# Performance work log

Hardware: AMD Instinct MI355X
Metric: run time of the kernel (lower is better)

## Reference

```python
import jax, jax.numpy as jnp
import numpy as np

INV_SQRT_2 = 0.7071067811865476


def setup_inputs() -> dict:
    key = jax.random.key(0)
    k1, k2, k3, k4, k5 = jax.random.split(key, 5)
    batch, nodes, edges, dim_in, dim_out = 2, 10000, 320000, 64, 64
    x = jax.random.normal(k1, (batch, nodes, dim_in, 3), dtype=jnp.float32)
    src = jax.random.randint(k2, (edges,), 0, nodes, dtype=jnp.int32)
    dst = jax.random.randint(k3, (edges,), 0, nodes, dtype=jnp.int32)
    # VecLinear weights (no bias; equivariant linear over the channel dim)
    W_src = jax.random.normal(k4, (dim_out, dim_in), dtype=jnp.float32) / np.sqrt(dim_in)
    W_dst = jax.random.normal(k5, (dim_out, dim_in), dtype=jnp.float32) / np.sqrt(dim_in)
    return {"x": x, "W_src": W_src, "W_dst": W_dst, "src": src, "dst": dst}


def reference(x, W_src, W_dst, src, dst):
    # x: (b, nodes, dim_in, 3); gather node feats per edge, mix channels, combine.
    xs = jnp.take(x, src, axis=1)  # (b, edges, dim_in, 3)
    xd = jnp.take(x, dst, axis=1)  # (b, edges, dim_in, 3)
    ys = jnp.einsum('oi,beiv->beov', W_src, xs)
    yd = jnp.einsum('oi,beiv->beov', W_dst, xd)
    return (ys + yd) * INV_SQRT_2  # (b, edges, dim_out, 3)
```

## Files before the change

kernel.cpp:

```cpp
#include <hip/hip_runtime.h>

#define INV_SQRT_2F 0.70710678118654752440f

typedef float fvec4 __attribute__((ext_vector_type(4)));

static __device__ __forceinline__ unsigned short f2bf(float f)
{
    unsigned int u = __float_as_uint(f);
    u += 0x7fffu + ((u >> 16) & 1u);
    return (unsigned short)(u >> 16);
}

static __device__ __forceinline__ fvec4 combine4(uint2 a, uint2 b)
{
    fvec4 r;
    r.x = (__uint_as_float(a.x << 16)         + __uint_as_float(b.x << 16))         * INV_SQRT_2F;
    r.y = (__uint_as_float(a.x & 0xffff0000u) + __uint_as_float(b.x & 0xffff0000u)) * INV_SQRT_2F;
    r.z = (__uint_as_float(a.y << 16)         + __uint_as_float(b.y << 16))         * INV_SQRT_2F;
    r.w = (__uint_as_float(a.y & 0xffff0000u) + __uint_as_float(b.y & 0xffff0000u)) * INV_SQRT_2F;
    return r;
}

__global__ void pack_sd(const int* __restrict__ src,
                        const int* __restrict__ dst,
                        unsigned int* __restrict__ sd, int edges)
{
    int i = blockIdx.x * blockDim.x + threadIdx.x;
    int stride = gridDim.x * blockDim.x;
    for (; i < edges; i += stride)
        sd[i] = ((unsigned int)src[i] << 16) | (unsigned int)dst[i];
}

__global__ void __launch_bounds__(128)
node_transform(const float* __restrict__ x,
               const float* __restrict__ W_src,
               const float* __restrict__ W_dst,
               unsigned short* __restrict__ y_src,
               unsigned short* __restrict__ y_dst,
               int nodes, int bn_total)
{
    __shared__ float xs[192];
    int bn = blockIdx.x;
    if (bn >= bn_total) return;
    int b = bn / nodes;
    int n = bn - b * nodes;

    const float4* xp = (const float4*)(x + (size_t)bn * 192);
    int t = threadIdx.x;
    if (t < 48) ((float4*)xs)[t] = xp[t];
    __syncthreads();

    int o = t & 63;
    const float*    W = (t < 64) ? W_src : W_dst;
    unsigned short* y = (t < 64) ? y_src : y_dst;

    const float4* Wrow = (const float4*)(W + o * 64);
    float a0 = 0.f, a1 = 0.f, a2 = 0.f;
#pragma unroll
    for (int i4 = 0; i4 < 16; ++i4) {
        float4 w = Wrow[i4];
        int i = i4 * 4;
        a0 = fmaf(w.x, xs[(i + 0) * 3 + 0], a0);
        a1 = fmaf(w.x, xs[(i + 0) * 3 + 1], a1);
        a2 = fmaf(w.x, xs[(i + 0) * 3 + 2], a2);
        a0 = fmaf(w.y, xs[(i + 1) * 3 + 0], a0);
        a1 = fmaf(w.y, xs[(i + 1) * 3 + 1], a1);
        a2 = fmaf(w.y, xs[(i + 1) * 3 + 2], a2);
        a0 = fmaf(w.z, xs[(i + 2) * 3 + 0], a0);
        a1 = fmaf(w.z, xs[(i + 2) * 3 + 1], a1);
        a2 = fmaf(w.z, xs[(i + 2) * 3 + 2], a2);
        a0 = fmaf(w.w, xs[(i + 3) * 3 + 0], a0);
        a1 = fmaf(w.w, xs[(i + 3) * 3 + 1], a1);
        a2 = fmaf(w.w, xs[(i + 3) * 3 + 2], a2);
    }
    unsigned short* yp = y + ((size_t)n * 2 + b) * 192 + o * 3;
    yp[0] = f2bf(a0);
    yp[1] = f2bf(a1);
    yp[2] = f2bf(a2);
}

__global__ void __launch_bounds__(256)
edge_combine2(const unsigned short* __restrict__ y_src,
              const unsigned short* __restrict__ y_dst,
              const unsigned int* __restrict__ sd,
              float* __restrict__ out,
              int edges)
{
    const int half   = edges >> 1;
    const int total  = half * 48;
    const int stride = gridDim.x * blockDim.x;
    const uint2* ys = (const uint2*)y_src;
    const uint2* yd = (const uint2*)y_dst;
    fvec4*       o4 = (fvec4*)out;

    for (int t = blockIdx.x * blockDim.x + threadIdx.x; t < total; t += stride) {
        int e0 = t / 48;
        int j  = t - e0 * 48;
        int e1 = e0 + half;

        unsigned int p0 = sd[e0];
        unsigned int p1 = sd[e1];
        size_t s0 = (size_t)(p0 >> 16)      * 96 + j;
        size_t d0 = (size_t)(p0 & 0xffffu)  * 96 + j;
        size_t s1 = (size_t)(p1 >> 16)      * 96 + j;
        size_t d1 = (size_t)(p1 & 0xffffu)  * 96 + j;

        uint2 a00 = ys[s0];
        uint2 b00 = yd[d0];
        uint2 a01 = ys[s0 + 48];
        uint2 b01 = yd[d0 + 48];
        uint2 a10 = ys[s1];
        uint2 b10 = yd[d1];
        uint2 a11 = ys[s1 + 48];
        uint2 b11 = yd[d1 + 48];

        __builtin_nontemporal_store(combine4(a00, b00), &o4[(size_t)e0 * 48 + j]);
        __builtin_nontemporal_store(combine4(a01, b01), &o4[((size_t)edges + e0) * 48 + j]);
        __builtin_nontemporal_store(combine4(a10, b10), &o4[(size_t)e1 * 48 + j]);
        __builtin_nontemporal_store(combine4(a11, b11), &o4[((size_t)edges + e1) * 48 + j]);
    }
}

__global__ void edge_combine_last(const unsigned short* __restrict__ y_src,
                                  const unsigned short* __restrict__ y_dst,
                                  const unsigned int* __restrict__ sd,
                                  float* __restrict__ out,
                                  int edges)
{
    int j = threadIdx.x;
    int e = edges - 1;
    const uint2* ys = (const uint2*)y_src;
    const uint2* yd = (const uint2*)y_dst;
    fvec4*       o4 = (fvec4*)out;
    unsigned int p = sd[e];
    size_t s = (size_t)(p >> 16)     * 96 + j;
    size_t d = (size_t)(p & 0xffffu) * 96 + j;
    uint2 a0 = ys[s];
    uint2 b0 = yd[d];
    uint2 a1 = ys[s + 48];
    uint2 b1 = yd[d + 48];
    __builtin_nontemporal_store(combine4(a0, b0), &o4[(size_t)e * 48 + j]);
    __builtin_nontemporal_store(combine4(a1, b1), &o4[((size_t)edges + e) * 48 + j]);
}

__global__ void __launch_bounds__(256)
edge_combine(const unsigned short* __restrict__ y_src,
             const unsigned short* __restrict__ y_dst,
             const int* __restrict__ src,
             const int* __restrict__ dst,
             float* __restrict__ out,
             int edges)
{
    const int total  = edges * 48;
    const int stride = gridDim.x * blockDim.x;
    const uint2* ys = (const uint2*)y_src;
    const uint2* yd = (const uint2*)y_dst;
    fvec4*       o4 = (fvec4*)out;

    for (int t = blockIdx.x * blockDim.x + threadIdx.x; t < total; t += stride) {
        int e = t / 48;
        int j = t - e * 48;
        size_t sb = (size_t)src[e] * 96 + j;
        size_t db = (size_t)dst[e] * 96 + j;

        uint2 a0 = ys[sb];
        uint2 b0 = yd[db];
        uint2 a1 = ys[sb + 48];
        uint2 b1 = yd[db + 48];

        __builtin_nontemporal_store(combine4(a0, b0), &o4[(size_t)e * 48 + j]);
        __builtin_nontemporal_store(combine4(a1, b1), &o4[((size_t)edges + e) * 48 + j]);
    }
}

__global__ void __launch_bounds__(64)
edge_fused(const float* __restrict__ x,
           const float* __restrict__ W_src,
           const float* __restrict__ W_dst,
           const int* __restrict__ src,
           const int* __restrict__ dst,
           float* __restrict__ out,
           int edges, int nodes)
{
    __shared__ float xs[192];
    __shared__ float xd[192];
    int be = blockIdx.x;
    int b  = be / edges;
    int e  = be - b * edges;
    int s  = src[e];
    int d  = dst[e];
    const float* xps = x + ((size_t)b * nodes + s) * 192;
    const float* xpd = x + ((size_t)b * nodes + d) * 192;
    int t = threadIdx.x;
#pragma unroll
    for (int k = 0; k < 3; ++k) {
        xs[t + 64 * k] = xps[t + 64 * k];
        xd[t + 64 * k] = xpd[t + 64 * k];
    }
    __syncthreads();
    float a0 = 0.f, a1 = 0.f, a2 = 0.f;
#pragma unroll
    for (int i = 0; i < 64; ++i) {
        float ws = W_src[t * 64 + i];
        float wd = W_dst[t * 64 + i];
        a0 += ws * xs[i * 3 + 0] + wd * xd[i * 3 + 0];
        a1 += ws * xs[i * 3 + 1] + wd * xd[i * 3 + 1];
        a2 += ws * xs[i * 3 + 2] + wd * xd[i * 3 + 2];
    }
    float* op = out + ((size_t)b * edges + e) * 192 + t * 3;
    op[0] = a0 * INV_SQRT_2F;
    op[1] = a1 * INV_SQRT_2F;
    op[2] = a2 * INV_SQRT_2F;
}

extern "C" void kernel_launch(void* const* d_in, const int* in_sizes, int n_in,
                              void* d_out, int out_size, void* d_ws, size_t ws_size,
                              hipStream_t stream)
{
    const float* x     = (const float*)d_in[0];
    const float* W_src = (const float*)d_in[1];
    const float* W_dst = (const float*)d_in[2];
    const int*   src   = (const int*)d_in[3];
    const int*   dst   = (const int*)d_in[4];
    float*       out   = (float*)d_out;

    const int batch = 2;
    const int edges = in_sizes[3];
    const int nodes = in_sizes[0] / (batch * 192);

    const size_t y_elems = (size_t)batch * nodes * 192;
    const size_t y_bytes = ((y_elems * 2 + 255) / 256) * 256;
    const size_t sd_bytes = (((size_t)edges * 4 + 255) / 256) * 256;
    const size_t needed_packed = 2 * y_bytes + sd_bytes;
    const size_t needed_plain  = 2 * y_bytes;

    char* wsb = (char*)d_ws;
    const int bn_total = batch * nodes;

    if (ws_size >= needed_packed && nodes <= 65535) {
        unsigned short* y_src = (unsigned short*)wsb;
        unsigned short* y_dst = (unsigned short*)(wsb + y_bytes);
        unsigned int*   sd    = (unsigned int*)(wsb + 2 * y_bytes);

        node_transform<<<bn_total, 128, 0, stream>>>(x, W_src, W_dst,
                                                     y_src, y_dst, nodes, bn_total);
        int egrid = (edges + 255) / 256; if (egrid > 1024) egrid = 1024;
        pack_sd<<<egrid, 256, 0, stream>>>(src, dst, sd, edges);
        edge_combine2<<<2048, 256, 0, stream>>>(y_src, y_dst, sd, out, edges);
        if (edges & 1)
            edge_combine_last<<<1, 48, 0, stream>>>(y_src, y_dst, sd, out, edges);
    } else if (ws_size >= needed_plain) {
        unsigned short* y_src = (unsigned short*)wsb;
        unsigned short* y_dst = (unsigned short*)(wsb + y_bytes);
        node_transform<<<bn_total, 128, 0, stream>>>(x, W_src, W_dst,
                                                     y_src, y_dst, nodes, bn_total);
        edge_combine<<<2048, 256, 0, stream>>>(y_src, y_dst, src, dst, out, edges);
    } else {
        edge_fused<<<batch * edges, 64, 0, stream>>>(x, W_src, W_dst,
                                                     src, dst, out, edges, nodes);
    }
}
```

Before: 211.3 us.

## Split src/dst gathers across lane pairs with 16-byte loads and shuffle exchange

Reworks the edge combine kernel so each thread handles four edges and loads only the src or the dst row (chosen by lane parity) with 16-byte loads. Neighbouring lanes swap halves through __shfl_xor so each still combines its src and dst values. The aim is wider, better-coalesced gather transactions and more memory-level parallelism per thread. The cost is extra cross-lane shuffles and a generalized tail kernel for edge counts not divisible by four.

```diff
diff --git a/kernel.cpp b/kernel.cpp
--- a/kernel.cpp
+++ b/kernel.cpp
@@ -18,6 +18,14 @@
     r.y = (__uint_as_float(a.x & 0xffff0000u) + __uint_as_float(b.x & 0xffff0000u)) * INV_SQRT_2F;
     r.z = (__uint_as_float(a.y << 16)         + __uint_as_float(b.y << 16))         * INV_SQRT_2F;
     r.w = (__uint_as_float(a.y & 0xffff0000u) + __uint_as_float(b.y & 0xffff0000u)) * INV_SQRT_2F;
+    return r;
+}
+
+static __device__ __forceinline__ uint2 xchg1(uint2 v)
+{
+    uint2 r;
+    r.x = __shfl_xor((unsigned int)v.x, 1);
+    r.y = __shfl_xor((unsigned int)v.y, 1);
     return r;
 }
 
@@ -80,55 +88,65 @@
 }
 
 __global__ void __launch_bounds__(256)
-edge_combine2(const unsigned short* __restrict__ y_src,
-              const unsigned short* __restrict__ y_dst,
-              const unsigned int* __restrict__ sd,
-              float* __restrict__ out,
-              int edges)
-{
-    const int half   = edges >> 1;
-    const int total  = half * 48;
+edge_combine_p(const unsigned short* __restrict__ y_src,
+               const unsigned short* __restrict__ y_dst,
+               const unsigned int* __restrict__ sd,
+               float* __restrict__ out,
+               int edges)
+{
+    const int Q = edges >> 2;
+    const int total = Q * 48;
     const int stride = gridDim.x * blockDim.x;
-    const uint2* ys = (const uint2*)y_src;
-    const uint2* yd = (const uint2*)y_dst;
-    fvec4*       o4 = (fvec4*)out;
+    const uint4* ys4 = (const uint4*)y_src;
+    const uint4* yd4 = (const uint4*)y_dst;
+    fvec4*       o4  = (fvec4*)out;
 
     for (int t = blockIdx.x * blockDim.x + threadIdx.x; t < total; t += stride) {
-        int e0 = t / 48;
-        int j  = t - e0 * 48;
-        int e1 = e0 + half;
-
-        unsigned int p0 = sd[e0];
-        unsigned int p1 = sd[e1];
-        size_t s0 = (size_t)(p0 >> 16)      * 96 + j;
-        size_t d0 = (size_t)(p0 & 0xffffu)  * 96 + j;
-        size_t s1 = (size_t)(p1 >> 16)      * 96 + j;
-        size_t d1 = (size_t)(p1 & 0xffffu)  * 96 + j;
-
-        uint2 a00 = ys[s0];
-        uint2 b00 = yd[d0];
-        uint2 a01 = ys[s0 + 48];
-        uint2 b01 = yd[d0 + 48];
-        uint2 a10 = ys[s1];
-        uint2 b10 = yd[d1];
-        uint2 a11 = ys[s1 + 48];
-        uint2 b11 = yd[d1 + 48];
-
-        __builtin_nontemporal_store(combine4(a00, b00), &o4[(size_t)e0 * 48 + j]);
-        __builtin_nontemporal_store(combine4(a01, b01), &o4[((size_t)edges + e0) * 48 + j]);
-        __builtin_nontemporal_store(combine4(a10, b10), &o4[(size_t)e1 * 48 + j]);
-        __builtin_nontemporal_store(combine4(a11, b11), &o4[((size_t)edges + e1) * 48 + j]);
-    }
-}
-
-__global__ void edge_combine_last(const unsigned short* __restrict__ y_src,
+        int g  = t / 48;
+        int j  = t - g * 48;
+        int par = j & 1;
+        int jj  = j >> 1;
+
+        uint2 p01 = *(const uint2*)&sd[2 * g];
+        uint2 p23 = *(const uint2*)&sd[2 * Q + 2 * g];
+        unsigned int pk[4] = { p01.x, p01.y, p23.x, p23.y };
+        int ek[4] = { 2 * g, 2 * g + 1, 2 * Q + 2 * g, 2 * Q + 2 * g + 1 };
+
+        const uint4* base = par ? yd4 : ys4;
+
+#pragma unroll
+        for (int k = 0; k < 4; ++k) {
+            unsigned int row = par ? (pk[k] & 0xffffu) : (pk[k] >> 16);
+            const uint4* rp = base + (size_t)row * 48 + jj;
+            uint4 v0 = rp[0];
+            uint4 v1 = rp[24];
+
+            uint2 kept0 = par ? make_uint2(v0.z, v0.w) : make_uint2(v0.x, v0.y);
+            uint2 send0 = par ? make_uint2(v0.x, v0.y) : make_uint2(v0.z, v0.w);
+            uint2 recv0 = xchg1(send0);
+            __builtin_nontemporal_store(combine4(kept0, recv0),
+                                        &o4[(size_t)ek[k] * 48 + j]);
+
+            uint2 kept1 = par ? make_uint2(v1.z, v1.w) : make_uint2(v1.x, v1.y);
+            uint2 send1 = par ? make_uint2(v1.x, v1.y) : make_uint2(v1.z, v1.w);
+            uint2 recv1 = xchg1(send1);
+            __builtin_nontemporal_store(combine4(kept1, recv1),
+                                        &o4[((size_t)edges + ek[k]) * 48 + j]);
+        }
+    }
+}
+
+__global__ void edge_combine_tail(const unsigned short* __restrict__ y_src,
                                   const unsigned short* __restrict__ y_dst,
                                   const unsigned int* __restrict__ sd,
                                   float* __restrict__ out,
-                                  int edges)
-{
-    int j = threadIdx.x;
-    int e = edges - 1;
+                                  int edges, int e_begin)
+{
+    int idx = blockIdx.x * blockDim.x + threadIdx.x;
+    int nt = (edges - e_begin) * 48;
+    if (idx >= nt) return;
+    int e = e_begin + idx / 48;
+    int j = idx - (idx / 48) * 48;
     const uint2* ys = (const uint2*)y_src;
     const uint2* yd = (const uint2*)y_dst;
     fvec4*       o4 = (fvec4*)out;
@@ -237,7 +255,7 @@
     char* wsb = (char*)d_ws;
     const int bn_total = batch * nodes;
 
-    if (ws_size >= needed_packed && nodes <= 65535) {
+    if (ws_size >= needed_packed && nodes <= 65535 && edges >= 4) {
         unsigned short* y_src = (unsigned short*)wsb;
         unsigned short* y_dst = (unsigned short*)(wsb + y_bytes);
         unsigned int*   sd    = (unsigned int*)(wsb + 2 * y_bytes);
@@ -246,9 +264,11 @@
                                                      y_src, y_dst, nodes, bn_total);
         int egrid = (edges + 255) / 256; if (egrid > 1024) egrid = 1024;
         pack_sd<<<egrid, 256, 0, stream>>>(src, dst, sd, edges);
-        edge_combine2<<<2048, 256, 0, stream>>>(y_src, y_dst, sd, out, edges);
-        if (edges & 1)
-            edge_combine_last<<<1, 48, 0, stream>>>(y_src, y_dst, sd, out, edges);
+        edge_combine_p<<<2048, 256, 0, stream>>>(y_src, y_dst, sd, out, edges);
+        int tail = edges & 3;
+        if (tail)
+            edge_combine_tail<<<1, 256, 0, stream>>>(y_src, y_dst, sd, out,
+                                                     edges, edges - tail);
     } else if (ws_size >= needed_plain) {
         unsigned short* y_src = (unsigned short*)wsb;
         unsigned short* y_dst = (unsigned short*)(wsb + y_bytes);
```

Measured after the change: 210.5 us, median of 2. About the same (-0.4%).

## Split node features into per-batch half-channel planes and gather them in phases

Applied to the files above, without the earlier changes.

The node transform now writes its bf16 output as four separate planes, one per (batch, output-channel half), each sized nodes x 32 channels x 3. The edge combine kernel walks these planes one at a time, so each phase gathers only from a plane of about 1.9 MB per input. The aim is to keep the randomly gathered rows resident in cache rather than spreading accesses over the whole node table. The cost is that each edge's index pair is re-read four times and output writes become 384-byte strided chunks instead of contiguous rows.

```diff
diff --git a/kernel.cpp b/kernel.cpp
--- a/kernel.cpp
+++ b/kernel.cpp
@@ -73,103 +73,77 @@
         a1 = fmaf(w.w, xs[(i + 3) * 3 + 1], a1);
         a2 = fmaf(w.w, xs[(i + 3) * 3 + 2], a2);
     }
-    unsigned short* yp = y + ((size_t)n * 2 + b) * 192 + o * 3;
+    int h = o >> 5;
+    int c = o & 31;
+    unsigned short* yp = y + (((size_t)(b * 2 + h) * nodes + n) * 96) + c * 3;
     yp[0] = f2bf(a0);
     yp[1] = f2bf(a1);
     yp[2] = f2bf(a2);
 }
 
 __global__ void __launch_bounds__(256)
-edge_combine2(const unsigned short* __restrict__ y_src,
-              const unsigned short* __restrict__ y_dst,
-              const unsigned int* __restrict__ sd,
-              float* __restrict__ out,
-              int edges)
-{
-    const int half   = edges >> 1;
-    const int total  = half * 48;
+edge_combine_phased(const unsigned short* __restrict__ y_src,
+                    const unsigned short* __restrict__ y_dst,
+                    const unsigned int* __restrict__ sd,
+                    float* __restrict__ out,
+                    int edges, int nodes)
+{
+    const int total  = edges * 96;
     const int stride = gridDim.x * blockDim.x;
     const uint2* ys = (const uint2*)y_src;
     const uint2* yd = (const uint2*)y_dst;
     fvec4*       o4 = (fvec4*)out;
 
     for (int t = blockIdx.x * blockDim.x + threadIdx.x; t < total; t += stride) {
-        int e0 = t / 48;
-        int j  = t - e0 * 48;
-        int e1 = e0 + half;
-
-        unsigned int p0 = sd[e0];
-        unsigned int p1 = sd[e1];
-        size_t s0 = (size_t)(p0 >> 16)      * 96 + j;
-        size_t d0 = (size_t)(p0 & 0xffffu)  * 96 + j;
-        size_t s1 = (size_t)(p1 >> 16)      * 96 + j;
-        size_t d1 = (size_t)(p1 & 0xffffu)  * 96 + j;
-
-        uint2 a00 = ys[s0];
-        uint2 b00 = yd[d0];
-        uint2 a01 = ys[s0 + 48];
-        uint2 b01 = yd[d0 + 48];
-        uint2 a10 = ys[s1];
-        uint2 b10 = yd[d1];
-        uint2 a11 = ys[s1 + 48];
-        uint2 b11 = yd[d1 + 48];
-
-        __builtin_nontemporal_store(combine4(a00, b00), &o4[(size_t)e0 * 48 + j]);
-        __builtin_nontemporal_store(combine4(a01, b01), &o4[((size_t)edges + e0) * 48 + j]);
-        __builtin_nontemporal_store(combine4(a10, b10), &o4[(size_t)e1 * 48 + j]);
-        __builtin_nontemporal_store(combine4(a11, b11), &o4[((size_t)edges + e1) * 48 + j]);
-    }
-}
-
-__global__ void edge_combine_last(const unsigned short* __restrict__ y_src,
-                                  const unsigned short* __restrict__ y_dst,
-                                  const unsigned int* __restrict__ sd,
-                                  float* __restrict__ out,
-                                  int edges)
-{
-    int j = threadIdx.x;
-    int e = edges - 1;
-    const uint2* ys = (const uint2*)y_src;
-    const uint2* yd = (const uint2*)y_dst;
-    fvec4*       o4 = (fvec4*)out;
-    unsigned int p = sd[e];
-    size_t s = (size_t)(p >> 16)     * 96 + j;
-    size_t d = (size_t)(p & 0xffffu) * 96 + j;
-    uint2 a0 = ys[s];
-    uint2 b0 = yd[d];
-    uint2 a1 = ys[s + 48];
-    uint2 b1 = yd[d + 48];
-    __builtin_nontemporal_store(combine4(a0, b0), &o4[(size_t)e * 48 + j]);
-    __builtin_nontemporal_store(combine4(a1, b1), &o4[((size_t)edges + e) * 48 + j]);
+        int pe = t / 24;
+        int j  = t - pe * 24;
+        int p  = pe / edges;
+        int e  = pe - p * edges;
+
+        unsigned int q = __builtin_nontemporal_load(&sd[e]);
+        unsigned int srow = q >> 16;
+        unsigned int drow = q & 0xffffu;
+
+        uint2 a = ys[((size_t)p * nodes + srow) * 24 + j];
+        uint2 b = yd[((size_t)p * nodes + drow) * 24 + j];
+
+        int bb = p >> 1;
+        int h  = p & 1;
+        size_t ob = ((size_t)bb * edges + e) * 48 + h * 24 + j;
+        __builtin_nontemporal_store(combine4(a, b), &o4[ob]);
+    }
 }
 
 __global__ void __launch_bounds__(256)
-edge_combine(const unsigned short* __restrict__ y_src,
-             const unsigned short* __restrict__ y_dst,
-             const int* __restrict__ src,
-             const int* __restrict__ dst,
-             float* __restrict__ out,
-             int edges)
-{
-    const int total  = edges * 48;
+edge_combine_phased_u(const unsigned short* __restrict__ y_src,
+                      const unsigned short* __restrict__ y_dst,
+                      const int* __restrict__ src,
+                      const int* __restrict__ dst,
+                      float* __restrict__ out,
+                      int edges, int nodes)
+{
+    const int total  = edges * 96;
     const int stride = gridDim.x * blockDim.x;
     const uint2* ys = (const uint2*)y_src;
     const uint2* yd = (const uint2*)y_dst;
     fvec4*       o4 = (fvec4*)out;
 
     for (int t = blockIdx.x * blockDim.x + threadIdx.x; t < total; t += stride) {
-        int e = t / 48;
-        int j = t - e * 48;
-        size_t sb = (size_t)src[e] * 96 + j;
-        size_t db = (size_t)dst[e] * 96 + j;
-
-        uint2 a0 = ys[sb];
-        uint2 b0 = yd[db];
-        uint2 a1 = ys[sb + 48];
-        uint2 b1 = yd[db + 48];
-
-        __builtin_nontemporal_store(combine4(a0, b0), &o4[(size_t)e * 48 + j]);
-        __builtin_nontemporal_store(combine4(a1, b1), &o4[((size_t)edges + e) * 48 + j]);
+        int pe = t / 24;
+        int j  = t - pe * 24;
+        int p  = pe / edges;
+        int e  = pe - p * edges;
+
+        unsigned int srow = (unsigned int)__builtin_nontemporal_load(&src[e]);
+        unsigned int drow = (unsigned int)__builtin_nontemporal_load(&dst[e]);
+
+        uint2 a = ys[((size_t)p * nodes + srow) * 24 + j];
+        uint2 b = yd[((size_t)p * nodes + drow) * 24 + j];
+
+        int bb = p >> 1;
+        int h  = p & 1;
+        size_t ob = ((size_t)bb * edges + e) * 48 + h * 24 + j;
+        __builtin_nontemporal_store(combine4(a, b), &o4[ob]);
     }
 }
 
@@ -246,15 +220,15 @@
                                                      y_src, y_dst, nodes, bn_total);
         int egrid = (edges + 255) / 256; if (egrid > 1024) egrid = 1024;
         pack_sd<<<egrid, 256, 0, stream>>>(src, dst, sd, edges);
-        edge_combine2<<<2048, 256, 0, stream>>>(y_src, y_dst, sd, out, edges);
-        if (edges & 1)
-            edge_combine_last<<<1, 48, 0, stream>>>(y_src, y_dst, sd, out, edges);
+        edge_combine_phased<<<2048, 256, 0, stream>>>(y_src, y_dst, sd, out,
+                                                      edges, nodes);
     } else if (ws_size >= needed_plain) {
         unsigned short* y_src = (unsigned short*)wsb;
         unsigned short* y_dst = (unsigned short*)(wsb + y_bytes);
         node_transform<<<bn_total, 128, 0, stream>>>(x, W_src, W_dst,
                                                      y_src, y_dst, nodes, bn_total);
-        edge_combine<<<2048, 256, 0, stream>>>(y_src, y_dst, src, dst, out, edges);
+        edge_combine_phased_u<<<2048, 256, 0, stream>>>(y_src, y_dst, src, dst,
+                                                        out, edges, nodes);
     } else {
         edge_fused<<<batch * edges, 64, 0, stream>>>(x, W_src, W_dst,
                                                      src, dst, out, edges, nodes);
```

Measured after the change: 251.1 us. 18.8% more time.
